# Kernel optimization log

Hardware: AMD Instinct MI355X
Metric: run time of the kernel (lower is better)

## Reference

```python
import jax, jax.numpy as jnp
import numpy as np

EPS = 1e-12  # F.normalize eps


def _l2_normalize(x):
    n = jnp.sqrt(jnp.sum(x * x, axis=1, keepdims=True))
    return x / jnp.maximum(n, EPS)


def setup_inputs() -> dict:
    key = jax.random.key(0)
    k1, k2, k3 = jax.random.split(key, 3)
    N, B, D = 1024, 1024, 128
    return {
        "node_embedding": jax.random.normal(k1, (N, D), dtype=jnp.float32),
        "graph_embedding": jax.random.normal(k2, (B, D), dtype=jnp.float32),
        "graph_metric": jax.random.uniform(k3, (B, B), dtype=jnp.float32),
    }


def reference(node_embedding, graph_embedding, graph_metric):
    # L2 normalize (F.normalize p=2 dim=1)
    ne = _l2_normalize(node_embedding)   # [N, D]
    ge = _l2_normalize(graph_embedding)  # [B, D]
    N, D = ne.shape

    # pairwise concatenated embeddings: replaces the O(N^2) python loop of
    # torch.cat((ne[i], ne[j])) + stack with one broadcast-and-concat pass.
    left = jnp.broadcast_to(ne[:, None, :], (N, N, D))
    right = jnp.broadcast_to(ne[None, :, :], (N, N, D))
    pairwise_embeddings_matrix = jnp.concatenate([left, right], axis=-1).reshape(N * N, 2 * D)

    # node loss: 'CL' branch — cross entropy with identity soft labels.
    node_logits = ne @ ne.T  # [N, N]
    # -mean over rows of sum(eye * log_softmax) == -mean(diag(log_softmax))
    node_logp = jax.nn.log_softmax(node_logits, axis=1)
    node_loss = -jnp.mean(jnp.diagonal(node_logp))

    # graph loss: else branch — genGraphMetric ends with row softmax.
    gm = jax.nn.softmax(graph_metric, axis=-1)  # [B, B]
    graph_logits = ge @ ge.T                    # [B, B]
    lp = jax.nn.log_softmax(graph_logits, axis=1)
    lpT = jax.nn.log_softmax(graph_logits.T, axis=1)
    graph_loss = (-jnp.mean(jnp.sum(gm * lp, axis=1))
                  - jnp.mean(jnp.sum(gm.T * lpT, axis=1)))

    alpha = 0.5
    loss = alpha * node_loss + (1.0 - alpha) * graph_loss
    return (loss, node_loss, graph_loss, graph_logits, pairwise_embeddings_matrix)
```

## Files before the change

kernel.cpp:

```cpp
#include <hip/hip_runtime.h>
#include <math.h>

#define NN 1024
#define DD 128
#define BB 1024
#define TI 4
#define TJ 32

typedef float floatx4 __attribute__((ext_vector_type(4)));

__device__ __forceinline__ float waveReduceSum(float v) {
#pragma unroll
  for (int off = 32; off > 0; off >>= 1) v += __shfl_xor(v, off);
  return v;
}
__device__ __forceinline__ float waveReduceMax(float v) {
#pragma unroll
  for (int off = 32; off > 0; off >>= 1) v = fmaxf(v, __shfl_xor(v, off));
  return v;
}

__global__ __launch_bounds__(256) void prep_kernel(
    const float* __restrict__ ne, const float* __restrict__ ge,
    const float* __restrict__ gm, float* __restrict__ ne_n,
    float* __restrict__ ge_n, float* __restrict__ gm_max,
    float* __restrict__ gm_den) {
  int unit = blockIdx.x * 4 + (threadIdx.x >> 6);
  int lane = threadIdx.x & 63;
  if (unit < NN + BB) {
    const float* src;
    float* dst;
    if (unit < NN) { src = ne + (size_t)unit * DD; dst = ne_n + (size_t)unit * DD; }
    else { src = ge + (size_t)(unit - NN) * DD; dst = ge_n + (size_t)(unit - NN) * DD; }
    float2 v = ((const float2*)src)[lane];
    float ss = v.x * v.x + v.y * v.y;
    ss = waveReduceSum(ss);
    float scale = 1.0f / fmaxf(sqrtf(ss), 1e-12f);
    float2 o;
    o.x = v.x * scale;
    o.y = v.y * scale;
    ((float2*)dst)[lane] = o;
  } else {
    int row = unit - (NN + BB);
    const float4* r = (const float4*)(gm + (size_t)row * BB);
    float vals[16];
    float m = -INFINITY;
#pragma unroll
    for (int k = 0; k < 4; ++k) {
      float4 v = r[lane + 64 * k];
      vals[k * 4 + 0] = v.x; vals[k * 4 + 1] = v.y;
      vals[k * 4 + 2] = v.z; vals[k * 4 + 3] = v.w;
      m = fmaxf(m, fmaxf(fmaxf(v.x, v.y), fmaxf(v.z, v.w)));
    }
    m = waveReduceMax(m);
    float s = 0.f;
#pragma unroll
    for (int t = 0; t < 16; ++t) s += expf(vals[t] - m);
    s = waveReduceSum(s);
    if (lane == 0) { gm_max[row] = m; gm_den[row] = s; }
  }
}

__global__ __launch_bounds__(256) void fused_kernel(
    const float* __restrict__ nen, const float* __restrict__ gen,
    const float* __restrict__ gm, const float* __restrict__ gm_max,
    const float* __restrict__ gm_den, float* __restrict__ out_logits,
    float* __restrict__ outp, float* __restrict__ node_partial,
    float* __restrict__ graph_partial) {
  __shared__ __align__(16) char smem[19136];
  int b = blockIdx.x;
  int tid = threadIdx.x;
  int lane = tid & 63;
  int w = tid >> 6;
  int m5 = b % 5;

  if (m5 != 4) {
    int pwId = (b / 5) * 4 + m5;
    int bi = pwId >> 5, bj = pwId & 31;
    int I0 = bi * TI, J0 = bj * TJ;
    float (*SHI)[DD] = (float (*)[DD])smem;
    float (*SHJ)[DD] = (float (*)[DD])(smem + 2048);
    float* LJ0 = (float*)(smem + 18432);
    float* LI0 = (float*)(smem + 18560);
    float* LI0N = (float*)(smem + 18576);

#pragma unroll
    for (int p = 0; p < 5; ++p) {
      int task = tid + 256 * p;
      if (task < (TI + TJ) * 32) {
        int row = task >> 5;
        int c4 = task & 31;
        const float* src = (row < TI) ? nen + (size_t)(I0 + row) * DD
                                      : nen + (size_t)(J0 + row - TI) * DD;
        floatx4 A = *(const floatx4*)(src + 4 * c4);
        float nxt = __shfl_down(A.x, 1);
        floatx4 Sv;
        Sv.x = A.y; Sv.y = A.z; Sv.z = A.w; Sv.w = nxt;
        float* dst = (row < TI) ? &SHI[row][4 * c4] : &SHJ[row - TI][4 * c4];
        *(floatx4*)dst = Sv;
        if (c4 == 0) {
          if (row < TI) {
            LI0[row] = A.x;
            int nr = I0 + row + 1;
            if (nr > 1023) nr = 0;
            LI0N[row] = nen[(size_t)nr * DD];
          } else {
            LJ0[row - TI] = A.x;
          }
        }
      }
    }
    __syncthreads();

    bool is31 = (lane == 31);
    bool is63 = (lane == 63);
    bool patch = is31 | is63;
    bool lastSeg = (bj == 31) && (w == 3);
    bool tailThread = (pwId == 8191) && (tid == 255);

    for (int ic = 0; ic < TI; ++ic) {
      float li0 = LI0[ic];
      float li0n = LI0N[ic];
      size_t segf = (((size_t)(I0 + ic) << 10) + (size_t)J0) << 8;
      float* gb = outp + segf + 1 + 4 * tid;
#pragma unroll
      for (int q = 0; q < 8; ++q) {
        int jc = w + 4 * q;
        const float* addr = (lane < 32) ? &SHI[ic][4 * lane]
                                        : &SHJ[jc][4 * (lane - 32)];
        floatx4 v = *(const floatx4*)addr;
        float lj0 = LJ0[jc];
        float spec = is31 ? lj0 : ((lastSeg && q == 7) ? li0n : li0);
        v.w = patch ? spec : v.w;
        if (tailThread && ic == TI - 1 && q == 7) {
          gb[0] = v.x; gb[1] = v.y; gb[2] = v.z;
        } else {
          *(floatx4*)gb = v;
        }
        gb += 1024;
      }
    }
    if (pwId == 0 && tid == 0) outp[0] = nen[0];
    return;
  }

  int lossId = b / 5;
  float* q = (float*)smem;
  float* logits = q + DD;
  float* red = logits + NN;
  int g = lane >> 4, gl = lane & 15;

  if (lossId < 1024) {
    int i = lossId;
    if (tid < DD) q[tid] = nen[(size_t)i * DD + tid];
    __syncthreads();
    const float4* qv = (const float4*)q;
    float4 b0 = qv[gl * 2], b1 = qv[gl * 2 + 1];
#pragma unroll 4
    for (int p = 0; p < 64; ++p) {
      int j = p * 16 + w * 4 + g;
      const float4* rowp = (const float4*)(nen + (size_t)j * DD);
      float4 a0 = rowp[gl * 2], a1 = rowp[gl * 2 + 1];
      float acc = a0.x * b0.x + a0.y * b0.y + a0.z * b0.z + a0.w * b0.w +
                  a1.x * b1.x + a1.y * b1.y + a1.z * b1.z + a1.w * b1.w;
      acc += __shfl_xor(acc, 1);
      acc += __shfl_xor(acc, 2);
      acc += __shfl_xor(acc, 4);
      acc += __shfl_xor(acc, 8);
      if (gl == 0) logits[j] = acc;
    }
    __syncthreads();
    float lv[4];
    float m = -INFINITY;
#pragma unroll
    for (int k = 0; k < 4; ++k) {
      lv[k] = logits[tid + 256 * k];
      m = fmaxf(m, lv[k]);
    }
    m = waveReduceMax(m);
    if (lane == 0) red[w] = m;
    __syncthreads();
    float M = fmaxf(fmaxf(red[0], red[1]), fmaxf(red[2], red[3]));
    float s = 0.f;
#pragma unroll
    for (int k = 0; k < 4; ++k) s += expf(lv[k] - M);
    s = waveReduceSum(s);
    if (lane == 0) red[4 + w] = s;
    __syncthreads();
    float S = red[4] + red[5] + red[6] + red[7];
    if (tid == 0) node_partial[i] = logits[i] - (M + logf(S));
  } else {
    int i = lossId - 1024;
    if (tid < DD) q[tid] = gen[(size_t)i * DD + tid];
    __syncthreads();
    const float4* qv = (const float4*)q;
    float4 b0 = qv[gl * 2], b1 = qv[gl * 2 + 1];
#pragma unroll 4
    for (int p = 0; p < 64; ++p) {
      int j = p * 16 + w * 4 + g;
      const float4* rowp = (const float4*)(gen + (size_t)j * DD);
      float4 a0 = rowp[gl * 2], a1 = rowp[gl * 2 + 1];
      float acc = a0.x * b0.x + a0.y * b0.y + a0.z * b0.z + a0.w * b0.w +
                  a1.x * b1.x + a1.y * b1.y + a1.z * b1.z + a1.w * b1.w;
      acc += __shfl_xor(acc, 1);
      acc += __shfl_xor(acc, 2);
      acc += __shfl_xor(acc, 4);
      acc += __shfl_xor(acc, 8);
      if (gl == 0) logits[j] = acc;
    }
    __syncthreads();
    float lv[4];
    float m = -INFINITY;
#pragma unroll
    for (int k = 0; k < 4; ++k) {
      lv[k] = logits[tid + 256 * k];
      m = fmaxf(m, lv[k]);
      out_logits[(size_t)i * BB + tid + 256 * k] = lv[k];
    }
    m = waveReduceMax(m);
    if (lane == 0) red[w] = m;
    __syncthreads();
    float M = fmaxf(fmaxf(red[0], red[1]), fmaxf(red[2], red[3]));
    float s = 0.f;
#pragma unroll
    for (int k = 0; k < 4; ++k) s += expf(lv[k] - M);
    s = waveReduceSum(s);
    if (lane == 0) red[4 + w] = s;
    __syncthreads();
    float S = red[4] + red[5] + red[6] + red[7];
    float lse = M + logf(S);
    float gmx_i = gm_max[i];
    float inv_i = 1.0f / gm_den[i];
    float c = 0.f;
#pragma unroll
    for (int k = 0; k < 4; ++k) {
      int j = tid + 256 * k;
      float lp = lv[k] - lse;
      float wij = expf(gm[(size_t)i * BB + j] - gmx_i) * inv_i;
      float wji = expf(gm[(size_t)j * BB + i] - gm_max[j]) / gm_den[j];
      c += (wij + wji) * lp;
    }
    c = waveReduceSum(c);
    __syncthreads();
    if (lane == 0) red[w] = c;
    __syncthreads();
    if (tid == 0) graph_partial[i] = red[0] + red[1] + red[2] + red[3];
  }
}

__global__ __launch_bounds__(256) void final_kernel(
    const float* __restrict__ node_partial,
    const float* __restrict__ graph_partial, float* __restrict__ out) {
  int tid = threadIdx.x;
  int lane = tid & 63, wid = tid >> 6;
  __shared__ float red[8];
  float ns = 0.f, gs = 0.f;
#pragma unroll
  for (int k = 0; k < 4; ++k) {
    ns += node_partial[tid + 256 * k];
    gs += graph_partial[tid + 256 * k];
  }
  ns = waveReduceSum(ns);
  gs = waveReduceSum(gs);
  if (lane == 0) { red[wid] = ns; red[4 + wid] = gs; }
  __syncthreads();
  if (tid == 0) {
    float nsum = red[0] + red[1] + red[2] + red[3];
    float gsum = red[4] + red[5] + red[6] + red[7];
    float node_loss = -nsum / (float)NN;
    float graph_loss = -gsum / (float)BB;
    float loss = 0.5f * node_loss + 0.5f * graph_loss;
    out[0] = loss;
    out[1] = node_loss;
    out[2] = graph_loss;
  }
}

extern "C" void kernel_launch(void* const* d_in, const int* in_sizes, int n_in,
                              void* d_out, int out_size, void* d_ws,
                              size_t ws_size, hipStream_t stream) {
  const float* ne = (const float*)d_in[0];
  const float* ge = (const float*)d_in[1];
  const float* gm = (const float*)d_in[2];
  float* out = (float*)d_out;
  float* ws = (float*)d_ws;

  float* ne_n = ws;
  float* ge_n = ws + 131072;
  float* gm_max = ws + 262144;
  float* gm_den = ws + 263168;
  float* node_partial = ws + 264192;
  float* graph_partial = ws + 265216;

  float* out_logits = out + 3;
  float* out_pair = out + 3 + (size_t)NN * NN;

  hipLaunchKernelGGL(prep_kernel, dim3((NN + 2 * BB) / 4), dim3(256), 0,
                     stream, ne, ge, gm, ne_n, ge_n, gm_max, gm_den);
  hipLaunchKernelGGL(fused_kernel, dim3(10240), dim3(256), 0, stream,
                     ne_n, ge_n, gm, gm_max, gm_den, out_logits,
                     out_pair, node_partial, graph_partial);
  hipLaunchKernelGGL(final_kernel, dim3(1), dim3(256), 0, stream,
                     node_partial, graph_partial, out);
}
```

Before: 240.2 us.

## Process four query rows per loss block and re-interleave grid at 16:1

Each loss block now computes logits for four query rows at once, so every key row loaded from global memory is reused across four dot products instead of one. This cuts loss blocks from 2048 to 512, and the block interleaving with pairwise-copy blocks changes from 4:1 to 16:1. The cost is more shared memory per block (16KB of logits) and a serial per-row softmax with extra barriers, which may reduce occupancy and make loss blocks long-running stragglers.

Result: slower. 279.5 us (+16.4%).

```diff
diff --git a/kernel.cpp b/kernel.cpp
--- a/kernel.cpp
+++ b/kernel.cpp
@@ -72,10 +72,10 @@
   int tid = threadIdx.x;
   int lane = tid & 63;
   int w = tid >> 6;
-  int m5 = b % 5;
-
-  if (m5 != 4) {
-    int pwId = (b / 5) * 4 + m5;
+  int g17 = b / 17, r17 = b % 17;
+
+  if (r17 != 8) {
+    int pwId = g17 * 16 + (r17 < 8 ? r17 : r17 - 1);
     int bi = pwId >> 5, bj = pwId & 31;
     int I0 = bi * TI, J0 = bj * TJ;
     float (*SHI)[DD] = (float (*)[DD])smem;
@@ -144,107 +144,103 @@
     return;
   }
 
-  int lossId = b / 5;
-  float* q = (float*)smem;
-  float* logits = q + DD;
-  float* red = logits + NN;
+  int lossId = g17;
+  bool isNode = (lossId < 256);
+  int i0 = (isNode ? lossId : lossId - 256) * 4;
+  const float* X = isNode ? nen : gen;
+  float* ql = (float*)smem;
+  float* logits = ql + 512;
+  float* red = logits + 4096;
   int g = lane >> 4, gl = lane & 15;
 
-  if (lossId < 1024) {
-    int i = lossId;
-    if (tid < DD) q[tid] = nen[(size_t)i * DD + tid];
-    __syncthreads();
-    const float4* qv = (const float4*)q;
-    float4 b0 = qv[gl * 2], b1 = qv[gl * 2 + 1];
-#pragma unroll 4
-    for (int p = 0; p < 64; ++p) {
-      int j = p * 16 + w * 4 + g;
-      const float4* rowp = (const float4*)(nen + (size_t)j * DD);
-      float4 a0 = rowp[gl * 2], a1 = rowp[gl * 2 + 1];
+  ((float2*)ql)[tid] = ((const float2*)(X + (size_t)i0 * DD))[tid];
+  __syncthreads();
+
+  const float4* qv = (const float4*)ql;
+#pragma unroll 2
+  for (int p = 0; p < 64; ++p) {
+    int j = p * 16 + w * 4 + g;
+    const float4* rowp = (const float4*)(X + (size_t)j * DD);
+    float4 a0 = rowp[gl * 2], a1 = rowp[gl * 2 + 1];
+#pragma unroll
+    for (int ic = 0; ic < 4; ++ic) {
+      float4 b0 = qv[ic * 32 + gl * 2], b1 = qv[ic * 32 + gl * 2 + 1];
       float acc = a0.x * b0.x + a0.y * b0.y + a0.z * b0.z + a0.w * b0.w +
                   a1.x * b1.x + a1.y * b1.y + a1.z * b1.z + a1.w * b1.w;
       acc += __shfl_xor(acc, 1);
       acc += __shfl_xor(acc, 2);
       acc += __shfl_xor(acc, 4);
       acc += __shfl_xor(acc, 8);
-      if (gl == 0) logits[j] = acc;
-    }
-    __syncthreads();
-    float lv[4];
-    float m = -INFINITY;
-#pragma unroll
-    for (int k = 0; k < 4; ++k) {
-      lv[k] = logits[tid + 256 * k];
-      m = fmaxf(m, lv[k]);
-    }
-    m = waveReduceMax(m);
-    if (lane == 0) red[w] = m;
-    __syncthreads();
-    float M = fmaxf(fmaxf(red[0], red[1]), fmaxf(red[2], red[3]));
-    float s = 0.f;
-#pragma unroll
-    for (int k = 0; k < 4; ++k) s += expf(lv[k] - M);
-    s = waveReduceSum(s);
-    if (lane == 0) red[4 + w] = s;
-    __syncthreads();
-    float S = red[4] + red[5] + red[6] + red[7];
-    if (tid == 0) node_partial[i] = logits[i] - (M + logf(S));
+      if (gl == 0) logits[ic * 1024 + j] = acc;
+    }
+  }
+  __syncthreads();
+
+  if (isNode) {
+    for (int ic = 0; ic < 4; ++ic) {
+      int i = i0 + ic;
+      float lv[4];
+      float m = -INFINITY;
+#pragma unroll
+      for (int k = 0; k < 4; ++k) {
+        lv[k] = logits[ic * 1024 + tid + 256 * k];
+        m = fmaxf(m, lv[k]);
+      }
+      m = waveReduceMax(m);
+      if (lane == 0) red[w] = m;
+      __syncthreads();
+      float M = fmaxf(fmaxf(red[0], red[1]), fmaxf(red[2], red[3]));
+      float s = 0.f;
+#pragma unroll
+      for (int k = 0; k < 4; ++k) s += expf(lv[k] - M);
+      s = waveReduceSum(s);
+      if (lane == 0) red[4 + w] = s;
+      __syncthreads();
+      float S = red[4] + red[5] + red[6] + red[7];
+      if (tid == 0) node_partial[i] = logits[ic * 1024 + i] - (M + logf(S));
+      __syncthreads();
+    }
   } else {
-    int i = lossId - 1024;
-    if (tid < DD) q[tid] = gen[(size_t)i * DD + tid];
-    __syncthreads();
-    const float4* qv = (const float4*)q;
-    float4 b0 = qv[gl * 2], b1 = qv[gl * 2 + 1];
-#pragma unroll 4
-    for (int p = 0; p < 64; ++p) {
-      int j = p * 16 + w * 4 + g;
-      const float4* rowp = (const float4*)(gen + (size_t)j * DD);
-      float4 a0 = rowp[gl * 2], a1 = rowp[gl * 2 + 1];
-      float acc = a0.x * b0.x + a0.y * b0.y + a0.z * b0.z + a0.w * b0.w +
-                  a1.x * b1.x + a1.y * b1.y + a1.z * b1.z + a1.w * b1.w;
-      acc += __shfl_xor(acc, 1);
-      acc += __shfl_xor(acc, 2);
-      acc += __shfl_xor(acc, 4);
-      acc += __shfl_xor(acc, 8);
-      if (gl == 0) logits[j] = acc;
-    }
-    __syncthreads();
-    float lv[4];
-    float m = -INFINITY;
-#pragma unroll
-    for (int k = 0; k < 4; ++k) {
-      lv[k] = logits[tid + 256 * k];
-      m = fmaxf(m, lv[k]);
-      out_logits[(size_t)i * BB + tid + 256 * k] = lv[k];
-    }
-    m = waveReduceMax(m);
-    if (lane == 0) red[w] = m;
-    __syncthreads();
-    float M = fmaxf(fmaxf(red[0], red[1]), fmaxf(red[2], red[3]));
-    float s = 0.f;
-#pragma unroll
-    for (int k = 0; k < 4; ++k) s += expf(lv[k] - M);
-    s = waveReduceSum(s);
-    if (lane == 0) red[4 + w] = s;
-    __syncthreads();
-    float S = red[4] + red[5] + red[6] + red[7];
-    float lse = M + logf(S);
-    float gmx_i = gm_max[i];
-    float inv_i = 1.0f / gm_den[i];
-    float c = 0.f;
-#pragma unroll
-    for (int k = 0; k < 4; ++k) {
-      int j = tid + 256 * k;
-      float lp = lv[k] - lse;
-      float wij = expf(gm[(size_t)i * BB + j] - gmx_i) * inv_i;
-      float wji = expf(gm[(size_t)j * BB + i] - gm_max[j]) / gm_den[j];
-      c += (wij + wji) * lp;
-    }
-    c = waveReduceSum(c);
-    __syncthreads();
-    if (lane == 0) red[w] = c;
-    __syncthreads();
-    if (tid == 0) graph_partial[i] = red[0] + red[1] + red[2] + red[3];
+    for (int ic = 0; ic < 4; ++ic) {
+      int i = i0 + ic;
+      float lv[4];
+      float m = -INFINITY;
+#pragma unroll
+      for (int k = 0; k < 4; ++k) {
+        lv[k] = logits[ic * 1024 + tid + 256 * k];
+        m = fmaxf(m, lv[k]);
+        out_logits[(size_t)i * BB + tid + 256 * k] = lv[k];
+      }
+      m = waveReduceMax(m);
+      if (lane == 0) red[w] = m;
+      __syncthreads();
+      float M = fmaxf(fmaxf(red[0], red[1]), fmaxf(red[2], red[3]));
+      float s = 0.f;
+#pragma unroll
+      for (int k = 0; k < 4; ++k) s += expf(lv[k] - M);
+      s = waveReduceSum(s);
+      if (lane == 0) red[4 + w] = s;
+      __syncthreads();
+      float S = red[4] + red[5] + red[6] + red[7];
+      float lse = M + logf(S);
+      float gmx_i = gm_max[i];
+      float inv_i = 1.0f / gm_den[i];
+      float c = 0.f;
+#pragma unroll
+      for (int k = 0; k < 4; ++k) {
+        int j = tid + 256 * k;
+        float lp = lv[k] - lse;
+        float wij = expf(gm[(size_t)i * BB + j] - gmx_i) * inv_i;
+        float wji = expf(gm[(size_t)j * BB + i] - gm_max[j]) / gm_den[j];
+        c += (wij + wji) * lp;
+      }
+      c = waveReduceSum(c);
+      __syncthreads();
+      if (lane == 0) red[w] = c;
+      __syncthreads();
+      if (tid == 0) graph_partial[i] = red[0] + red[1] + red[2] + red[3];
+      __syncthreads();
+    }
   }
 }
 
@@ -297,7 +293,7 @@
 
   hipLaunchKernelGGL(prep_kernel, dim3((NN + 2 * BB) / 4), dim3(256), 0,
                      stream, ne, ge, gm, ne_n, ge_n, gm_max, gm_den);
-  hipLaunchKernelGGL(fused_kernel, dim3(10240), dim3(256), 0, stream,
+  hipLaunchKernelGGL(fused_kernel, dim3(8704), dim3(256), 0, stream,
                      ne_n, ge_n, gm, gm_max, gm_den, out_logits,
                      out_pair, node_partial, graph_partial);
   hipLaunchKernelGGL(final_kernel, dim3(1), dim3(256), 0, stream,
```
